# Kernel optimization log

Measured on AMD Instinct MI355X. Metric: run time of the kernel, lower is better.

## Reference

```python
import jax, jax.numpy as jnp
import numpy as np

D = 256
K = 64


def setup_inputs() -> dict:
    key = jax.random.key(0)
    k1, k2, k3 = jax.random.split(key, 3)
    B, H, W = 16, 96, 96
    X = jax.random.normal(k1, (B, D, H, W), dtype=jnp.float32)
    std1 = 1.0 / float(np.sqrt(K * D))
    std2 = 1.0 / float(np.sqrt(K))
    codewords = jax.random.uniform(k2, (K, D), dtype=jnp.float32, minval=-std1, maxval=std1)
    scale = jax.random.uniform(k3, (K,), dtype=jnp.float32, minval=-std2, maxval=std2)
    return {"X": X, "codewords": codewords, "scale": scale}


def reference(X, codewords, scale):
    # X: [B, D, H, W] -> Xf: [B, N, D]
    B = X.shape[0]
    Xf = X.reshape(B, X.shape[1], -1).transpose(0, 2, 1)
    # Scaled L2 distances: SL[b,n,k] = scale[k] * ||x_bn - c_k||^2
    x2 = jnp.sum(Xf * Xf, axis=-1, keepdims=True)          # [B, N, 1]
    c2 = jnp.sum(codewords * codewords, axis=-1)            # [K]
    xc = jnp.einsum('bnd,kd->bnk', Xf, codewords)           # [B, N, K]
    SL = scale * (x2 - 2.0 * xc + c2)                       # [B, N, K]
    # Assignment weights: softmax over codewords K
    A = jax.nn.softmax(SL, axis=-1)                         # [B, N, K]
    # Aggregate residuals: E[b,k,d] = sum_n A[b,n,k] * (X[b,n,d] - C[k,d])
    E = jnp.einsum('bnk,bnd->bkd', A, Xf) - jnp.sum(A, axis=1)[:, :, None] * codewords
    return E
```

## Files before the change

### kernel.cpp

```cpp
#include <hip/hip_runtime.h>

#define NDIM  256
#define NK    64
#define NPIX  9216
#define NB    16
#define TN    64
#define NW    32
#define GRID  (NB*NW)

typedef _Float16 half2_t __attribute__((ext_vector_type(2)));
typedef _Float16 half4_t __attribute__((ext_vector_type(4)));
typedef _Float16 half8_t __attribute__((ext_vector_type(8)));
typedef float    f32x4  __attribute__((ext_vector_type(4)));

__device__ __forceinline__ float fdot2(half2_t a, half2_t b, float c) {
  return __builtin_amdgcn_fdot2(a, b, c, false);
}

#define BAR() asm volatile("s_waitcnt lgkmcnt(0)\n\ts_barrier" ::: "memory")

#define OFF_ASUM   0
#define OFF_APART  (NB * NK)
#define OFF_EPART  (OFF_APART + GRID * NK)
#define WS_NEED    ((size_t)OFF_EPART * 4 + (size_t)GRID * NK * NDIM * 2)

__global__ __launch_bounds__(256, 2) void encode_main(
    const float* __restrict__ X, const float* __restrict__ Cw,
    const float* __restrict__ scale,
    void* __restrict__ Eout, float* __restrict__ Aout, int mode)
{
  __shared__ _Float16 XbS[2][32 * 66 * 8];
  __shared__ _Float16 Al[NK][72];
  __shared__ float red2[4][TN];
  __shared__ float redM[4][TN];
  __shared__ float redS[4][TN];

  const int tid  = threadIdx.x;
  const int w    = __builtin_amdgcn_readfirstlane(tid >> 6);
  const int lane = tid & 63;
  const int m    = lane & 15, quad = lane >> 4;
  const int b    = blockIdx.x >> 5;
  const int wid  = blockIdx.x & 31;
  const int ntiles = (wid < 16) ? 5 : 4;
  const int pix0   = (wid * 4 + (wid < 16 ? wid : 16)) * TN;
  const float* Xbase = X + (size_t)b * NDIM * NPIX;
  const int kbase = w * 16;

  float xv[64];
  {
    const float* Xg = Xbase + (size_t)(w * 64) * NPIX + pix0 + lane;
#pragma unroll
    for (int i = 0; i < 64; ++i) xv[i] = Xg[(size_t)i * NPIX];
  }

  {
    const int kk = tid >> 2, ch = tid & 3;
    const float* Cr = Cw + kk * NDIM + ch * 64;
    float s = 0.f;
#pragma unroll
    for (int j = 0; j < 16; ++j) {
      const float4 v = *(const float4*)(Cr + 4 * j);
      s += v.x * v.x + v.y * v.y + v.z * v.z + v.w * v.w;
    }
    redM[ch][kk] = s;
  }

  half8_t af1[8];
#pragma unroll
  for (int ks = 0; ks < 8; ++ks) {
    const float* ap = Cw + (kbase + m) * NDIM + ks * 32 + quad * 8;
    const float4 a0 = *(const float4*)(ap);
    const float4 a1 = *(const float4*)(ap + 4);
    half8_t h;
    h[0] = (_Float16)a0.x; h[1] = (_Float16)a0.y;
    h[2] = (_Float16)a0.z; h[3] = (_Float16)a0.w;
    h[4] = (_Float16)a1.x; h[5] = (_Float16)a1.y;
    h[6] = (_Float16)a1.z; h[7] = (_Float16)a1.w;
    af1[ks] = h;
    __builtin_amdgcn_sched_barrier(0);
  }

  const float4 scv = *(const float4*)(scale + kbase + quad * 4);
  const float sc[4] = {scv.x, scv.y, scv.z, scv.w};

  BAR();
  float sq[4];
#pragma unroll
  for (int r = 0; r < 4; ++r) {
    const int k = kbase + quad * 4 + r;
    const float c2k = redM[0][k] + redM[1][k] + redM[2][k] + redM[3][k];
    sq[r] = sc[r] * c2k;
  }

  f32x4 acc_e[4][4];
#pragma unroll
  for (int i = 0; i < 4; ++i)
#pragma unroll
    for (int j = 0; j < 4; ++j)
      acc_e[i][j] = (f32x4){0.f, 0.f, 0.f, 0.f};
  float asum_acc = 0.f;

  auto STAGE = [&](int bufi) {
    _Float16* Xb = XbS[bufi];
    float xsq = 0.f;
#pragma unroll
    for (int g = 0; g < 8; ++g) {
      half8_t hv;
#pragma unroll
      for (int i = 0; i < 8; ++i) {
        const float v = xv[g * 8 + i];
        hv[i] = (_Float16)v; xsq += v * v;
      }
      *(half8_t*)&Xb[((w * 8 + g) * 66 + lane) * 8] = hv;
    }
    red2[w][lane] = xsq;
  };
  auto ISSUE = [&](int t) {
    const float* Xg = Xbase + (size_t)(w * 64) * NPIX + pix0 + t * TN + lane;
#pragma unroll
    for (int i = 0; i < 64; ++i) xv[i] = Xg[(size_t)i * NPIX];
  };

  STAGE(0);
  ISSUE(1);
  BAR();

  for (int tt = 0; tt < ntiles; ++tt) {
    const _Float16* Xb = XbS[tt & 1];

    f32x4 accs[4];
#pragma unroll
    for (int nt = 0; nt < 4; ++nt) accs[nt] = (f32x4){0.f, 0.f, 0.f, 0.f};
    __builtin_amdgcn_s_setprio(1);
#pragma unroll
    for (int ks = 0; ks < 8; ++ks) {
#pragma unroll
      for (int nt = 0; nt < 4; ++nt) {
        const half8_t bf = *(const half8_t*)&Xb[((ks * 4 + quad) * 66 + nt * 16 + m) * 8];
        accs[nt] = __builtin_amdgcn_mfma_f32_16x16x32_f16(af1[ks], bf, accs[nt], 0, 0, 0);
      }
    }
    __builtin_amdgcn_s_setprio(0);

    float e[4][4], mw[4];
#pragma unroll
    for (int nt = 0; nt < 4; ++nt) {
      const int p = nt * 16 + m;
      const float x2p = red2[0][p] + red2[1][p] + red2[2][p] + red2[3][p];
      float L[4];
      float mx = -3.0e38f;
#pragma unroll
      for (int r = 0; r < 4; ++r) {
        L[r] = sc[r] * x2p - 2.f * sc[r] * accs[nt][r] + sq[r];
        mx = fmaxf(mx, L[r]);
      }
      mx = fmaxf(mx, __shfl_xor(mx, 16));
      mx = fmaxf(mx, __shfl_xor(mx, 32));
      float s = 0.f;
#pragma unroll
      for (int r = 0; r < 4; ++r) { e[nt][r] = __expf(L[r] - mx); s += e[nt][r]; }
      s += __shfl_xor(s, 16);
      s += __shfl_xor(s, 32);
      mw[nt] = mx;
      if (lane < 16) { redM[w][p] = mx; redS[w][p] = s; }
    }
    BAR();
#pragma unroll
    for (int nt = 0; nt < 4; ++nt) {
      const int p = nt * 16 + m;
      const float M = fmaxf(fmaxf(redM[0][p], redM[1][p]),
                            fmaxf(redM[2][p], redM[3][p]));
      const float T = redS[0][p] * __expf(redM[0][p] - M)
                    + redS[1][p] * __expf(redM[1][p] - M)
                    + redS[2][p] * __expf(redM[2][p] - M)
                    + redS[3][p] * __expf(redM[3][p] - M);
      const float norm = __expf(mw[nt] - M) / T;
#pragma unroll
      for (int r = 0; r < 4; ++r)
        Al[kbase + quad * 4 + r][p] = (_Float16)(e[nt][r] * norm);
    }
    BAR();

    __builtin_amdgcn_s_setprio(1);
#pragma unroll
    for (int ks = 0; ks < 2; ++ks) {
      half8_t ba[4];
#pragma unroll
      for (int kt = 0; kt < 4; ++kt)
        ba[kt] = *(const half8_t*)&Al[kt * 16 + m][ks * 32 + quad * 8];
#pragma unroll
      for (int dt = 0; dt < 4; ++dt) {
        const int c = w * 8 + dt * 2 + (m >> 3);
        const int dlow = m & 7;
        half8_t xa;
#pragma unroll
        for (int j = 0; j < 8; ++j)
          xa[j] = Xb[(c * 66 + ks * 32 + quad * 8 + j) * 8 + dlow];
#pragma unroll
        for (int kt = 0; kt < 4; ++kt)
          acc_e[dt][kt] = __builtin_amdgcn_mfma_f32_16x16x32_f16(xa, ba[kt], acc_e[dt][kt], 0, 0, 0);
      }
    }
    __builtin_amdgcn_s_setprio(0);

    {
      const half2_t one = {(_Float16)1.f, (_Float16)1.f};
      const int ka = kbase + (lane >> 2);
      const int pa = (lane & 3) * 16;
      float s = 0.f;
#pragma unroll
      for (int lc = 0; lc < 2; ++lc) {
        const half8_t sv = *(const half8_t*)&Al[ka][pa + lc * 8];
        s = fdot2(__builtin_shufflevector(sv, sv, 0, 1), one, s);
        s = fdot2(__builtin_shufflevector(sv, sv, 2, 3), one, s);
        s = fdot2(__builtin_shufflevector(sv, sv, 4, 5), one, s);
        s = fdot2(__builtin_shufflevector(sv, sv, 6, 7), one, s);
      }
      s += __shfl_xor(s, 1);
      s += __shfl_xor(s, 2);
      asum_acc += s;
    }

    if (tt + 1 < ntiles) {
      STAGE((tt + 1) & 1);
      if (tt + 2 < ntiles) ISSUE(tt + 2);
      BAR();
    }
  }

  BAR();
  _Float16* Et = XbS[0];
#pragma unroll
  for (int dt = 0; dt < 4; ++dt)
#pragma unroll
    for (int kt = 0; kt < 4; ++kt)
#pragma unroll
      for (int r = 0; r < 4; ++r) {
        const int k = kt * 16 + m;
        const int d = w * 64 + dt * 16 + quad * 4 + r;
        Et[k * 264 + d] = (_Float16)acc_e[dt][kt][r];
      }
  BAR();
  const int ko = tid >> 2, cq = tid & 3;
  if (mode) {
    _Float16* Ebk = (_Float16*)Eout + (size_t)blockIdx.x * (NK * NDIM);
#pragma unroll
    for (int g = 0; g < 8; ++g)
      *(half8_t*)&Ebk[ko * NDIM + cq * 64 + g * 8] =
          *(const half8_t*)&Et[ko * 264 + cq * 64 + g * 8];
    if ((lane & 3) == 0)
      Aout[blockIdx.x * NK + kbase + (lane >> 2)] = asum_acc;
  } else {
    float* Ebk = (float*)Eout + (size_t)b * (NK * NDIM);
#pragma unroll
    for (int g = 0; g < 64; ++g)
      atomicAdd(&Ebk[ko * NDIM + cq * 64 + g], (float)Et[ko * 264 + cq * 64 + g]);
    if ((lane & 3) == 0)
      atomicAdd(&Aout[b * NK + kbase + (lane >> 2)], asum_acc);
  }
}

__global__ void finalize_partials(const _Float16* __restrict__ EpartH,
                                  const float* __restrict__ Apart,
                                  const float* __restrict__ Cw,
                                  float* __restrict__ out) {
  const int g = blockIdx.x * 256 + threadIdx.x;
  const int i0 = g * 4;
  const int bb = i0 >> 14;
  const int o  = i0 & 16383;
  const int k  = o >> 8, d = i0 & 255;
  float a = 0.f;
#pragma unroll 8
  for (int w = 0; w < NW; ++w) a += Apart[(bb * NW + w) * NK + k];
  float s0 = 0.f, s1 = 0.f, s2 = 0.f, s3 = 0.f;
  const _Float16* base = EpartH + (((size_t)bb * NW) << 14) + o;
#pragma unroll 4
  for (int w = 0; w < NW; ++w) {
    const half4_t v = *(const half4_t*)(base + ((size_t)w << 14));
    s0 += (float)v[0]; s1 += (float)v[1];
    s2 += (float)v[2]; s3 += (float)v[3];
  }
  const float4 c0 = *(const float4*)(Cw + k * NDIM + d);
  float4 r0;
  r0.x = s0 - a * c0.x; r0.y = s1 - a * c0.y;
  r0.z = s2 - a * c0.z; r0.w = s3 - a * c0.w;
  *(float4*)(out + i0) = r0;
}

__global__ void finalize_atomic(const float* __restrict__ E_acc,
                                const float* __restrict__ asum,
                                const float* __restrict__ Cw,
                                float* __restrict__ out) {
  const int i = blockIdx.x * 256 + threadIdx.x;
  const int d = i & 255;
  const int k = (i >> 8) & 63;
  const int bb = i >> 14;
  out[i] = E_acc[i] - asum[bb * NK + k] * Cw[k * NDIM + d];
}

extern "C" void kernel_launch(void* const* d_in, const int* in_sizes, int n_in,
                              void* d_out, int out_size, void* d_ws, size_t ws_size,
                              hipStream_t stream) {
  const float* X     = (const float*)d_in[0];
  const float* Cw    = (const float*)d_in[1];
  const float* scale = (const float*)d_in[2];
  float* out = (float*)d_out;

  float* wsf = (float*)d_ws;
  float* asum  = wsf + OFF_ASUM;
  float* Apart = wsf + OFF_APART;

  if (ws_size >= WS_NEED) {
    _Float16* EpartH = (_Float16*)(wsf + OFF_EPART);
    encode_main<<<GRID, 256, 0, stream>>>(X, Cw, scale, EpartH, Apart, 1);
    finalize_partials<<<(NB*NK*NDIM)/(256*4), 256, 0, stream>>>(EpartH, Apart, Cw, out);
  } else {
    float* E_acc = wsf + OFF_APART;
    hipMemsetAsync(wsf, 0,
                   (size_t)(NB*NK + NB*NK*NDIM) * sizeof(float), stream);
    encode_main<<<GRID, 256, 0, stream>>>(X, Cw, scale, E_acc, asum, 0);
    finalize_atomic<<<(NB*NK*NDIM)/256, 256, 0, stream>>>(E_acc, asum, Cw, out);
  }
}
```

Baseline: 239.3 us.

## Fuse partial reduction into main kernel via per-batch flag barrier

Removes the separate finalize kernel launch by having each block publish a per-call nonce-tagged flag after writing its fp16 partials. Block thread 0 then spins until all 32 blocks of the same batch have published, and each block reduces its 512-element slice of the output. This saves one kernel launch and the gap between kernels, but relies on all blocks of a batch being co-resident (512 blocks at 2 per CU) to avoid deadlock. It also adds spin-wait latency at the tail.

```diff
diff --git a/kernel.cpp b/kernel.cpp
--- a/kernel.cpp
+++ b/kernel.cpp
@@ -1,4 +1,5 @@
 #include <hip/hip_runtime.h>
+#include <stdint.h>
 
 #define NDIM  256
 #define NK    64
@@ -22,12 +23,15 @@
 #define OFF_ASUM   0
 #define OFF_APART  (NB * NK)
 #define OFF_EPART  (OFF_APART + GRID * NK)
-#define WS_NEED    ((size_t)OFF_EPART * 4 + (size_t)GRID * NK * NDIM * 2)
+#define OFF_FLAG   (OFF_EPART + (GRID * NK * NDIM) / 2)
+#define WS_NEED    ((size_t)(OFF_FLAG + GRID * 2) * 4)
 
 __global__ __launch_bounds__(256, 2) void encode_main(
     const float* __restrict__ X, const float* __restrict__ Cw,
     const float* __restrict__ scale,
-    void* __restrict__ Eout, float* __restrict__ Aout, int mode)
+    void* __restrict__ Eout, float* __restrict__ Aout,
+    uint32_t* __restrict__ flags, float* __restrict__ out,
+    uint32_t nonce, int mode)
 {
   __shared__ _Float16 XbS[2][32 * 66 * 8];
   __shared__ _Float16 Al[NK][72];
@@ -250,6 +254,50 @@
           *(const half8_t*)&Et[ko * 264 + cq * 64 + g * 8];
     if ((lane & 3) == 0)
       Aout[blockIdx.x * NK + kbase + (lane >> 2)] = asum_acc;
+
+    __syncthreads();
+    if (tid == 0) {
+      __threadfence();
+      const uint32_t idx = blockIdx.x;
+      uint32_t* f = flags + 2 * idx;
+      __hip_atomic_store(f,     0x9E3779B9u ^ idx ^ nonce, __ATOMIC_RELEASE,
+                         __HIP_MEMORY_SCOPE_AGENT);
+      __hip_atomic_store(f + 1, 0x85EBCA6Bu + idx + nonce, __ATOMIC_RELEASE,
+                         __HIP_MEMORY_SCOPE_AGENT);
+#pragma unroll 1
+      for (int w2 = 0; w2 < NW; ++w2) {
+        const uint32_t j = (uint32_t)(b * NW + w2);
+        uint32_t* fj = flags + 2 * j;
+        const uint32_t m0 = 0x9E3779B9u ^ j ^ nonce;
+        const uint32_t m1 = 0x85EBCA6Bu + j + nonce;
+        while (__hip_atomic_load(fj, __ATOMIC_RELAXED, __HIP_MEMORY_SCOPE_AGENT) != m0 ||
+               __hip_atomic_load(fj + 1, __ATOMIC_RELAXED, __HIP_MEMORY_SCOPE_AGENT) != m1)
+          __builtin_amdgcn_s_sleep(4);
+      }
+    }
+    __syncthreads();
+    __threadfence();
+
+    if (tid < 128) {
+      const int o  = wid * 512 + tid * 4;
+      const int k  = o >> 8, d = o & 255;
+      float a = 0.f;
+#pragma unroll 8
+      for (int w2 = 0; w2 < NW; ++w2) a += Aout[(b * NW + w2) * NK + k];
+      float s0 = 0.f, s1 = 0.f, s2 = 0.f, s3 = 0.f;
+      const _Float16* base = (const _Float16*)Eout + (((size_t)b * NW) << 14) + o;
+#pragma unroll 4
+      for (int w2 = 0; w2 < NW; ++w2) {
+        const half4_t v = *(const half4_t*)(base + ((size_t)w2 << 14));
+        s0 += (float)v[0]; s1 += (float)v[1];
+        s2 += (float)v[2]; s3 += (float)v[3];
+      }
+      const float4 c0 = *(const float4*)(Cw + k * NDIM + d);
+      float4 r0;
+      r0.x = s0 - a * c0.x; r0.y = s1 - a * c0.y;
+      r0.z = s2 - a * c0.z; r0.w = s3 - a * c0.w;
+      *(float4*)(out + (size_t)b * (NK * NDIM) + o) = r0;
+    }
   } else {
     float* Ebk = (float*)Eout + (size_t)b * (NK * NDIM);
 #pragma unroll
@@ -258,33 +306,6 @@
     if ((lane & 3) == 0)
       atomicAdd(&Aout[b * NK + kbase + (lane >> 2)], asum_acc);
   }
-}
-
-__global__ void finalize_partials(const _Float16* __restrict__ EpartH,
-                                  const float* __restrict__ Apart,
-                                  const float* __restrict__ Cw,
-                                  float* __restrict__ out) {
-  const int g = blockIdx.x * 256 + threadIdx.x;
-  const int i0 = g * 4;
-  const int bb = i0 >> 14;
-  const int o  = i0 & 16383;
-  const int k  = o >> 8, d = i0 & 255;
-  float a = 0.f;
-#pragma unroll 8
-  for (int w = 0; w < NW; ++w) a += Apart[(bb * NW + w) * NK + k];
-  float s0 = 0.f, s1 = 0.f, s2 = 0.f, s3 = 0.f;
-  const _Float16* base = EpartH + (((size_t)bb * NW) << 14) + o;
-#pragma unroll 4
-  for (int w = 0; w < NW; ++w) {
-    const half4_t v = *(const half4_t*)(base + ((size_t)w << 14));
-    s0 += (float)v[0]; s1 += (float)v[1];
-    s2 += (float)v[2]; s3 += (float)v[3];
-  }
-  const float4 c0 = *(const float4*)(Cw + k * NDIM + d);
-  float4 r0;
-  r0.x = s0 - a * c0.x; r0.y = s1 - a * c0.y;
-  r0.z = s2 - a * c0.z; r0.w = s3 - a * c0.w;
-  *(float4*)(out + i0) = r0;
 }
 
 __global__ void finalize_atomic(const float* __restrict__ E_acc,
@@ -310,15 +331,19 @@
   float* asum  = wsf + OFF_ASUM;
   float* Apart = wsf + OFF_APART;
 
+  static uint32_t nonce = 0x1234567u;
+  nonce += 0x9E3779B9u;
   if (ws_size >= WS_NEED) {
     _Float16* EpartH = (_Float16*)(wsf + OFF_EPART);
-    encode_main<<<GRID, 256, 0, stream>>>(X, Cw, scale, EpartH, Apart, 1);
-    finalize_partials<<<(NB*NK*NDIM)/(256*4), 256, 0, stream>>>(EpartH, Apart, Cw, out);
+    uint32_t* flags  = (uint32_t*)(wsf + OFF_FLAG);
+    encode_main<<<GRID, 256, 0, stream>>>(X, Cw, scale, EpartH, Apart,
+                                          flags, out, nonce, 1);
   } else {
     float* E_acc = wsf + OFF_APART;
     hipMemsetAsync(wsf, 0,
                    (size_t)(NB*NK + NB*NK*NDIM) * sizeof(float), stream);
-    encode_main<<<GRID, 256, 0, stream>>>(X, Cw, scale, E_acc, asum, 0);
+    encode_main<<<GRID, 256, 0, stream>>>(X, Cw, scale, E_acc, asum,
+                                          nullptr, out, nonce, 0);
     finalize_atomic<<<(NB*NK*NDIM)/256, 256, 0, stream>>>(E_acc, asum, Cw, out);
   }
 }
```

New measurement: 361.9 us. 1.51x slower.
